# Kernel optimization log

Hardware: AMD Instinct MI355X
Metric: run time of the kernel (lower is better)

The kernel has to match this reference:

```python
import jax, jax.numpy as jnp
import numpy as np

B, T, D = 16, 2048, 64


def setup_inputs() -> dict:
    key = jax.random.key(0)
    kq, kk, kv, kb = jax.random.split(key, 4)
    q = jax.random.normal(kq, (B, T, D), dtype=jnp.float32)
    k = jax.random.normal(kk, (B, T, D), dtype=jnp.float32)
    v = jax.random.normal(kv, (B, T, D), dtype=jnp.float32)
    add_attn = jax.random.normal(kb, (B, T, T), dtype=jnp.float32)
    return {"q": q, "k": k, "v": v, "add_attn": add_attn}


def reference(q, k, v, add_attn):
    # scale = 1/sqrt(head_dim), the standard value passed by callers
    scale = 1.0 / jnp.sqrt(jnp.asarray(q.shape[-1], dtype=q.dtype))
    # [B, T, T] attention logits: bmm(q, k^T) * scale + additive bias
    attn = jnp.einsum('btd,bsd->bts', q, k) * scale + add_attn
    # softmax over keys (dim=2); dropout p=0.0 is identity
    attn = jax.nn.softmax(attn, axis=2)
    # [B, T, D] weighted values
    output = jnp.einsum('bts,bsd->btd', attn, v)
    return (output, attn)
```

## Files before the change

kernel.cpp:

```cpp
#include <hip/hip_runtime.h>
#include <stdint.h>

#define NB 16
#define NT 2048
#define ND 64

typedef __attribute__((ext_vector_type(8))) short bf16x8;
typedef __attribute__((ext_vector_type(4))) float f32x4;
typedef __attribute__((ext_vector_type(4))) _Float16 f16x4;

__device__ __forceinline__ unsigned short f2bf(float f) {
    union { float f; unsigned u; } v; v.f = f;
    unsigned r = v.u + 0x7fffu + ((v.u >> 16) & 1u);
    return (unsigned short)(r >> 16);
}
__device__ __forceinline__ unsigned short f2h(float f) {
    union { _Float16 h; unsigned short u; } v; v.h = (_Float16)f; return v.u;
}

__global__ __launch_bounds__(256) void prep_k(const float* __restrict__ Q,
                                              const float* __restrict__ K,
                                              const float* __restrict__ V,
                                              unsigned short* __restrict__ qbf,
                                              unsigned short* __restrict__ kbf,
                                              unsigned short* __restrict__ vt)
{
    const size_t i = (size_t)blockIdx.x * 256 + threadIdx.x;
    const int which = blockIdx.y;
    if (which == 2) {
        float4 v4 = ((const float4*)V)[i];
        const int d4 = (int)(i & 15);
        const int t  = (int)((i >> 4) & (NT - 1));
        const int b  = (int)(i >> 15);
        unsigned short* base = vt + ((size_t)b * ND + d4 * 4) * NT + t;
        base[0]      = f2h(v4.x);
        base[NT]     = f2h(v4.y);
        base[2 * NT] = f2h(v4.z);
        base[3 * NT] = f2h(v4.w);
    } else {
        const float4* src = (which == 0) ? (const float4*)Q : (const float4*)K;
        unsigned short* dst = (which == 0) ? qbf : kbf;
        float4 v4 = src[i];
        union { unsigned short s[4]; unsigned long long ll; } u;
        u.s[0] = f2bf(v4.x); u.s[1] = f2bf(v4.y);
        u.s[2] = f2bf(v4.z); u.s[3] = f2bf(v4.w);
        *(unsigned long long*)(dst + 4 * i) = u.ll;
    }
}

__global__ __launch_bounds__(256, 2)
void attn_onepass(const unsigned short* __restrict__ qbf,
                  const unsigned short* __restrict__ kbf,
                  const unsigned short* __restrict__ vt,
                  const float* __restrict__ Bias,
                  float* __restrict__ Out,
                  float* __restrict__ Attn)
{
    const int b = blockIdx.y, q0 = blockIdx.x * 16;
    const int tid = threadIdx.x, w = tid >> 6, lane = tid & 63;
    const int n = lane & 15, qd = lane >> 4;
    const int kw0 = w * 512;

    __shared__ float s_rs[4][16];
    __shared__ float s_o[4 * 16 * 68];

    const unsigned short* qp = qbf + ((size_t)(b * NT + q0 + n)) * ND + qd * 8;
    const bf16x8 qf0 = *(const bf16x8*)qp;
    const bf16x8 qf1 = *(const bf16x8*)(qp + 32);
    const float* Bb = Bias + ((size_t)b * NT + q0 + n) * NT;
    float* Ab = Attn + ((size_t)b * NT + q0 + n) * NT;
    const unsigned short* vtb = vt + (size_t)b * ND * NT + (size_t)n * NT;

    f16x4 ev[32];
    float4 bb[4];
    bf16x8 kb0[2], kb1[2];
#pragma unroll
    for (int i = 0; i < 4; ++i)
        bb[i] = *(const float4*)(Bb + kw0 + 16 * i + qd * 4);
#pragma unroll
    for (int i = 0; i < 2; ++i) {
        const unsigned short* kp = kbf + ((size_t)(b * NT + kw0 + 16 * i + n)) * ND + qd * 8;
        kb0[i] = *(const bf16x8*)kp;
        kb1[i] = *(const bf16x8*)(kp + 32);
    }

    float rs = 0.f;
#pragma unroll
    for (int t = 0; t < 32; ++t) {
        const bf16x8 kf0 = kb0[t & 1];
        const bf16x8 kf1 = kb1[t & 1];
        const float4 bs = bb[t & 3];
        if (t + 2 < 32) {
            const unsigned short* kp =
                kbf + ((size_t)(b * NT + kw0 + 16 * (t + 2) + n)) * ND + qd * 8;
            kb0[t & 1] = *(const bf16x8*)kp;
            kb1[t & 1] = *(const bf16x8*)(kp + 32);
        }
        if (t + 4 < 32)
            bb[t & 3] = *(const float4*)(Bb + kw0 + 16 * (t + 4) + qd * 4);
        f32x4 acc = {0.f, 0.f, 0.f, 0.f};
        acc = __builtin_amdgcn_mfma_f32_16x16x32_bf16(kf0, qf0, acc, 0, 0, 0);
        acc = __builtin_amdgcn_mfma_f32_16x16x32_bf16(kf1, qf1, acc, 0, 0, 0);
        float e0 = __expf(__builtin_fmaf(acc[0], 0.125f, bs.x - 2.0f));
        float e1 = __expf(__builtin_fmaf(acc[1], 0.125f, bs.y - 2.0f));
        float e2 = __expf(__builtin_fmaf(acc[2], 0.125f, bs.z - 2.0f));
        float e3 = __expf(__builtin_fmaf(acc[3], 0.125f, bs.w - 2.0f));
        union { _Float16 h[4]; f16x4 v; } u;
        u.h[0] = (_Float16)e0; u.h[1] = (_Float16)e1;
        u.h[2] = (_Float16)e2; u.h[3] = (_Float16)e3;
        ev[t] = u.v;
        rs += (e0 + e1) + (e2 + e3);
    }

    f16x4 vc0[4], vc1[4];
#pragma unroll
    for (int dt = 0; dt < 4; ++dt) {
        const unsigned short* vp = vtb + kw0 + qd * 4 + (size_t)dt * 16 * NT;
        vc0[dt] = *(const f16x4*)(const void*)vp;
        vc1[dt] = *(const f16x4*)(const void*)(vp + 16);
    }

    rs += __shfl_xor(rs, 16, 64);
    rs += __shfl_xor(rs, 32, 64);
    if (lane < 16) s_rs[w][lane] = rs;
    __syncthreads();
    const float tot = (s_rs[0][n] + s_rs[1][n]) + (s_rs[2][n] + s_rs[3][n]);
    const float inv = 1.0f / tot;

    f32x4 oacc[4];
#pragma unroll
    for (int dt = 0; dt < 4; ++dt) oacc[dt] = (f32x4){0.f, 0.f, 0.f, 0.f};

#pragma unroll
    for (int tp = 0; tp < 16; ++tp) {
        const int key0 = kw0 + 32 * tp;
        f16x4 va0[4], va1[4];
#pragma unroll
        for (int dt = 0; dt < 4; ++dt) { va0[dt] = vc0[dt]; va1[dt] = vc1[dt]; }
        if (tp + 1 < 16) {
#pragma unroll
            for (int dt = 0; dt < 4; ++dt) {
                const unsigned short* vp =
                    vtb + key0 + 32 + qd * 4 + (size_t)dt * 16 * NT;
                vc0[dt] = *(const f16x4*)(const void*)vp;
                vc1[dt] = *(const f16x4*)(const void*)(vp + 16);
            }
        }
        const f16x4 e0v = ev[2 * tp];
        const f16x4 e1v = ev[2 * tp + 1];
        float4 s0, s1;
        s0.x = (float)e0v[0] * inv; s0.y = (float)e0v[1] * inv;
        s0.z = (float)e0v[2] * inv; s0.w = (float)e0v[3] * inv;
        s1.x = (float)e1v[0] * inv; s1.y = (float)e1v[1] * inv;
        s1.z = (float)e1v[2] * inv; s1.w = (float)e1v[3] * inv;
        *(float4*)(Ab + key0 + qd * 4) = s0;
        *(float4*)(Ab + key0 + 16 + qd * 4) = s1;
#pragma unroll
        for (int dt = 0; dt < 4; ++dt) {
            oacc[dt] = __builtin_amdgcn_mfma_f32_16x16x16f16(va0[dt], e0v, oacc[dt], 0, 0, 0);
            oacc[dt] = __builtin_amdgcn_mfma_f32_16x16x16f16(va1[dt], e1v, oacc[dt], 0, 0, 0);
        }
    }

#pragma unroll
    for (int dt = 0; dt < 4; ++dt) {
        float4 t4;
        t4.x = oacc[dt][0] * inv; t4.y = oacc[dt][1] * inv;
        t4.z = oacc[dt][2] * inv; t4.w = oacc[dt][3] * inv;
        *(float4*)&s_o[(w * 16 + n) * 68 + dt * 16 + qd * 4] = t4;
    }
    __syncthreads();
    {
        const int row = tid >> 4, d4 = (tid & 15) * 4;
        float4 o0 = *(const float4*)&s_o[(0 * 16 + row) * 68 + d4];
        float4 o1 = *(const float4*)&s_o[(1 * 16 + row) * 68 + d4];
        float4 o2 = *(const float4*)&s_o[(2 * 16 + row) * 68 + d4];
        float4 o3 = *(const float4*)&s_o[(3 * 16 + row) * 68 + d4];
        float4 o;
        o.x = (o0.x + o1.x) + (o2.x + o3.x);
        o.y = (o0.y + o1.y) + (o2.y + o3.y);
        o.z = (o0.z + o1.z) + (o2.z + o3.z);
        o.w = (o0.w + o1.w) + (o2.w + o3.w);
        *(float4*)(Out + ((size_t)b * NT + q0 + row) * ND + d4) = o;
    }
}

__device__ __forceinline__ bf16x8 pack8(float4 a, float4 b) {
    union { unsigned short s[8]; bf16x8 v; } u;
    u.s[0] = f2bf(a.x); u.s[1] = f2bf(a.y); u.s[2] = f2bf(a.z); u.s[3] = f2bf(a.w);
    u.s[4] = f2bf(b.x); u.s[5] = f2bf(b.y); u.s[6] = f2bf(b.z); u.s[7] = f2bf(b.w);
    return u.v;
}
__global__ __launch_bounds__(256, 2)
void attn_fused(const float* __restrict__ Q, const float* __restrict__ K,
                const float* __restrict__ V, const float* __restrict__ Bias,
                float* __restrict__ Out, float* __restrict__ Attn)
{
    const int b  = blockIdx.y;
    const int q0 = blockIdx.x * 16;
    const int tid  = threadIdx.x;
    const int w    = tid >> 6;
    const int lane = tid & 63;
    const int n  = lane & 15;
    const int qd = lane >> 4;
    const int kw0 = w * 512;
    __shared__ float s_rs[4][16];
    __shared__ __align__(16) unsigned char s_rp[4][16 * 80];
    const float* Qb = Q + ((size_t)b * NT + q0) * ND;
    const float* Kb = K + (size_t)b * NT * ND;
    const float* Vb = V + (size_t)b * NT * ND;
    const float* Bb = Bias + ((size_t)b * NT + q0) * NT;
    float* Ab = Attn + ((size_t)b * NT + q0) * NT;
    float* Ob = Out  + ((size_t)b * NT + q0) * ND;
    bf16x8 qf0, qf1;
    {
        const float* qp = Qb + n * ND + qd * 8;
        qf0 = pack8(*(const float4*)qp,        *(const float4*)(qp + 4));
        qf1 = pack8(*(const float4*)(qp + 32), *(const float4*)(qp + 36));
    }
    float ev[32][4];
    float rs = 0.f;
#pragma unroll
    for (int t = 0; t < 32; ++t) {
        const int key0 = kw0 + 16 * t;
        const float* kp = Kb + (size_t)(key0 + n) * ND + qd * 8;
        bf16x8 kf0 = pack8(*(const float4*)kp,        *(const float4*)(kp + 4));
        bf16x8 kf1 = pack8(*(const float4*)(kp + 32), *(const float4*)(kp + 36));
        f32x4 acc = {0.f, 0.f, 0.f, 0.f};
        acc = __builtin_amdgcn_mfma_f32_16x16x32_bf16(kf0, qf0, acc, 0, 0, 0);
        acc = __builtin_amdgcn_mfma_f32_16x16x32_bf16(kf1, qf1, acc, 0, 0, 0);
        float4 bs = *(const float4*)(Bb + (size_t)n * NT + key0 + qd * 4);
        float e0 = __expf(acc[0] * 0.125f + bs.x);
        float e1 = __expf(acc[1] * 0.125f + bs.y);
        float e2 = __expf(acc[2] * 0.125f + bs.z);
        float e3 = __expf(acc[3] * 0.125f + bs.w);
        ev[t][0] = e0; ev[t][1] = e1; ev[t][2] = e2; ev[t][3] = e3;
        rs += (e0 + e1) + (e2 + e3);
    }
    rs += __shfl_xor(rs, 16, 64);
    rs += __shfl_xor(rs, 32, 64);
    if (lane < 16) s_rs[w][lane] = rs;
    __syncthreads();
    const float tot = (s_rs[0][n] + s_rs[1][n]) + (s_rs[2][n] + s_rs[3][n]);
    const float inv = 1.0f / tot;
    f32x4 oacc[4];
#pragma unroll
    for (int dt = 0; dt < 4; ++dt) oacc[dt] = (f32x4){0.f, 0.f, 0.f, 0.f};
    unsigned char* rp = &s_rp[w][0];
#pragma unroll
    for (int c = 0; c < 16; ++c) {
        const int kbase = kw0 + 32 * c;
#pragma unroll
        for (int tt = 0; tt < 2; ++tt) {
            const int t = 2 * c + tt;
            float p0 = ev[t][0] * inv;
            float p1 = ev[t][1] * inv;
            float p2 = ev[t][2] * inv;
            float p3 = ev[t][3] * inv;
            float4 pv; pv.x = p0; pv.y = p1; pv.z = p2; pv.w = p3;
            *(float4*)(Ab + (size_t)n * NT + kbase + 16 * tt + qd * 4) = pv;
            union { unsigned short s[4]; unsigned long long ll; } pu;
            pu.s[0] = f2bf(p0); pu.s[1] = f2bf(p1);
            pu.s[2] = f2bf(p2); pu.s[3] = f2bf(p3);
            *(unsigned long long*)(rp + n * 80 + (16 * tt + 4 * qd) * 2) = pu.ll;
        }
        __syncthreads();
        bf16x8 pf;
        {
            union { uint4 u; bf16x8 v; } uu;
            uu.u = *(const uint4*)(rp + n * 80 + qd * 16);
            pf = uu.v;
        }
#pragma unroll
        for (int dt = 0; dt < 4; ++dt) {
            const int d = dt * 16 + n;
            const float* vp = Vb + (size_t)(kbase + qd * 8) * ND + d;
            float4 va, vb4;
            va.x  = vp[0];   va.y  = vp[64];  va.z  = vp[128]; va.w  = vp[192];
            vb4.x = vp[256]; vb4.y = vp[320]; vb4.z = vp[384]; vb4.w = vp[448];
            bf16x8 vf = pack8(va, vb4);
            oacc[dt] = __builtin_amdgcn_mfma_f32_16x16x32_bf16(vf, pf, oacc[dt], 0, 0, 0);
        }
        __syncthreads();
    }
#pragma unroll
    for (int dt = 0; dt < 4; ++dt)
#pragma unroll
        for (int r = 0; r < 4; ++r)
            atomicAdd(Ob + (size_t)n * ND + dt * 16 + qd * 4 + r, oacc[dt][r]);
}

extern "C" void kernel_launch(void* const* d_in, const int* in_sizes, int n_in,
                              void* d_out, int out_size, void* d_ws, size_t ws_size,
                              hipStream_t stream)
{
    const float* q    = (const float*)d_in[0];
    const float* k    = (const float*)d_in[1];
    const float* v    = (const float*)d_in[2];
    const float* bias = (const float*)d_in[3];
    float* out  = (float*)d_out;
    float* attn = out + (size_t)NB * NT * ND;

    const size_t elems = (size_t)NB * NT * ND;
    const size_t need  = 3 * elems * 2;

    if (ws_size >= need) {
        unsigned short* qbf = (unsigned short*)d_ws;
        unsigned short* kbf = qbf + elems;
        unsigned short* vtb = kbf + elems;
        prep_k<<<dim3((unsigned)(elems / 4 / 256), 3), 256, 0, stream>>>(q, k, v, qbf, kbf, vtb);
        attn_onepass<<<dim3(NT / 16, NB), 256, 0, stream>>>(qbf, kbf, vtb, bias, out, attn);
    } else {
        hipMemsetAsync(out, 0, (size_t)NB * NT * ND * sizeof(float), stream);
        dim3 grid(NT / 16, NB);
        attn_fused<<<grid, 256, 0, stream>>>(q, k, v, bias, out, attn);
    }
}
```

Before: 261.7 us.

## Split key range across 8 waves, remap blocks across XCDs, add sched barriers

Doubles the block to 512 threads, so each of 8 waves handles 256 keys instead of 512. This halves the per-thread exp and V register arrays and raises occupancy. Block indices are permuted so consecutive blocks spread across the 8 XCDs by batch, which changes L2 locality for K/V reuse. Explicit sched_barriers pin where the prefetch loads of K, bias and V sit, and V is now double-buffered two steps ahead. The cost is a larger shared-memory reduction across 8 waves, with half the threads idle in the final sum.

```diff
diff --git a/kernel.cpp b/kernel.cpp
--- a/kernel.cpp
+++ b/kernel.cpp
@@ -48,7 +48,7 @@
     }
 }
 
-__global__ __launch_bounds__(256, 2)
+__global__ __launch_bounds__(512, 4)
 void attn_onepass(const unsigned short* __restrict__ qbf,
                   const unsigned short* __restrict__ kbf,
                   const unsigned short* __restrict__ vt,
@@ -56,13 +56,17 @@
                   float* __restrict__ Out,
                   float* __restrict__ Attn)
 {
-    const int b = blockIdx.y, q0 = blockIdx.x * 16;
+    const int flat = blockIdx.x + (NT / 16) * blockIdx.y;
+    const int lin  = (flat & 7) * 256 + (flat >> 3);
+    const int b    = lin >> 7;
+    const int q0   = (lin & 127) * 16;
+
     const int tid = threadIdx.x, w = tid >> 6, lane = tid & 63;
     const int n = lane & 15, qd = lane >> 4;
-    const int kw0 = w * 512;
-
-    __shared__ float s_rs[4][16];
-    __shared__ float s_o[4 * 16 * 68];
+    const int kw0 = w * 256;
+
+    __shared__ float s_rs[8][16];
+    __shared__ float s_o[8 * 16 * 68];
 
     const unsigned short* qp = qbf + ((size_t)(b * NT + q0 + n)) * ND + qd * 8;
     const bf16x8 qf0 = *(const bf16x8*)qp;
@@ -70,34 +74,29 @@
     const float* Bb = Bias + ((size_t)b * NT + q0 + n) * NT;
     float* Ab = Attn + ((size_t)b * NT + q0 + n) * NT;
     const unsigned short* vtb = vt + (size_t)b * ND * NT + (size_t)n * NT;
-
-    f16x4 ev[32];
+    const unsigned short* kbp = kbf + ((size_t)(b * NT + kw0 + n)) * ND + qd * 8;
+    const float* bbp = Bb + kw0 + qd * 4;
+
+    f16x4 ev[16];
+    bf16x8 kb0[2], kb1[2];
     float4 bb[4];
-    bf16x8 kb0[2], kb1[2];
-#pragma unroll
-    for (int i = 0; i < 4; ++i)
-        bb[i] = *(const float4*)(Bb + kw0 + 16 * i + qd * 4);
 #pragma unroll
     for (int i = 0; i < 2; ++i) {
-        const unsigned short* kp = kbf + ((size_t)(b * NT + kw0 + 16 * i + n)) * ND + qd * 8;
+        const unsigned short* kp = kbp + (size_t)(16 * i) * ND;
         kb0[i] = *(const bf16x8*)kp;
         kb1[i] = *(const bf16x8*)(kp + 32);
     }
+#pragma unroll
+    for (int i = 0; i < 4; ++i)
+        bb[i] = *(const float4*)(bbp + 16 * i);
+    __builtin_amdgcn_sched_barrier(0);
 
     float rs = 0.f;
 #pragma unroll
-    for (int t = 0; t < 32; ++t) {
+    for (int t = 0; t < 16; ++t) {
         const bf16x8 kf0 = kb0[t & 1];
         const bf16x8 kf1 = kb1[t & 1];
         const float4 bs = bb[t & 3];
-        if (t + 2 < 32) {
-            const unsigned short* kp =
-                kbf + ((size_t)(b * NT + kw0 + 16 * (t + 2) + n)) * ND + qd * 8;
-            kb0[t & 1] = *(const bf16x8*)kp;
-            kb1[t & 1] = *(const bf16x8*)(kp + 32);
-        }
-        if (t + 4 < 32)
-            bb[t & 3] = *(const float4*)(Bb + kw0 + 16 * (t + 4) + qd * 4);
         f32x4 acc = {0.f, 0.f, 0.f, 0.f};
         acc = __builtin_amdgcn_mfma_f32_16x16x32_bf16(kf0, qf0, acc, 0, 0, 0);
         acc = __builtin_amdgcn_mfma_f32_16x16x32_bf16(kf1, qf1, acc, 0, 0, 0);
@@ -110,21 +109,34 @@
         u.h[2] = (_Float16)e2; u.h[3] = (_Float16)e3;
         ev[t] = u.v;
         rs += (e0 + e1) + (e2 + e3);
-    }
-
-    f16x4 vc0[4], vc1[4];
-#pragma unroll
-    for (int dt = 0; dt < 4; ++dt) {
-        const unsigned short* vp = vtb + kw0 + qd * 4 + (size_t)dt * 16 * NT;
-        vc0[dt] = *(const f16x4*)(const void*)vp;
-        vc1[dt] = *(const f16x4*)(const void*)(vp + 16);
-    }
+        __builtin_amdgcn_sched_barrier(0);
+        if (t + 2 < 16) {
+            const unsigned short* kp = kbp + (size_t)(16 * (t + 2)) * ND;
+            kb0[t & 1] = *(const bf16x8*)kp;
+            kb1[t & 1] = *(const bf16x8*)(kp + 32);
+        }
+        if (t + 4 < 16)
+            bb[t & 3] = *(const float4*)(bbp + 16 * (t + 4));
+        __builtin_amdgcn_sched_barrier(0);
+    }
+
+    f16x4 vr0[2][4], vr1[2][4];
+#pragma unroll
+    for (int i = 0; i < 2; ++i)
+#pragma unroll
+        for (int dt = 0; dt < 4; ++dt) {
+            const unsigned short* vp = vtb + kw0 + 32 * i + qd * 4 + (size_t)dt * 16 * NT;
+            vr0[i][dt] = *(const f16x4*)(const void*)vp;
+            vr1[i][dt] = *(const f16x4*)(const void*)(vp + 16);
+        }
+    __builtin_amdgcn_sched_barrier(0);
 
     rs += __shfl_xor(rs, 16, 64);
     rs += __shfl_xor(rs, 32, 64);
     if (lane < 16) s_rs[w][lane] = rs;
     __syncthreads();
-    const float tot = (s_rs[0][n] + s_rs[1][n]) + (s_rs[2][n] + s_rs[3][n]);
+    const float tot = ((s_rs[0][n] + s_rs[1][n]) + (s_rs[2][n] + s_rs[3][n])) +
+                      ((s_rs[4][n] + s_rs[5][n]) + (s_rs[6][n] + s_rs[7][n]));
     const float inv = 1.0f / tot;
 
     f32x4 oacc[4];
@@ -132,20 +144,8 @@
     for (int dt = 0; dt < 4; ++dt) oacc[dt] = (f32x4){0.f, 0.f, 0.f, 0.f};
 
 #pragma unroll
-    for (int tp = 0; tp < 16; ++tp) {
+    for (int tp = 0; tp < 8; ++tp) {
         const int key0 = kw0 + 32 * tp;
-        f16x4 va0[4], va1[4];
-#pragma unroll
-        for (int dt = 0; dt < 4; ++dt) { va0[dt] = vc0[dt]; va1[dt] = vc1[dt]; }
-        if (tp + 1 < 16) {
-#pragma unroll
-            for (int dt = 0; dt < 4; ++dt) {
-                const unsigned short* vp =
-                    vtb + key0 + 32 + qd * 4 + (size_t)dt * 16 * NT;
-                vc0[dt] = *(const f16x4*)(const void*)vp;
-                vc1[dt] = *(const f16x4*)(const void*)(vp + 16);
-            }
-        }
         const f16x4 e0v = ev[2 * tp];
         const f16x4 e1v = ev[2 * tp + 1];
         float4 s0, s1;
@@ -157,9 +157,20 @@
         *(float4*)(Ab + key0 + 16 + qd * 4) = s1;
 #pragma unroll
         for (int dt = 0; dt < 4; ++dt) {
-            oacc[dt] = __builtin_amdgcn_mfma_f32_16x16x16f16(va0[dt], e0v, oacc[dt], 0, 0, 0);
-            oacc[dt] = __builtin_amdgcn_mfma_f32_16x16x16f16(va1[dt], e1v, oacc[dt], 0, 0, 0);
-        }
+            oacc[dt] = __builtin_amdgcn_mfma_f32_16x16x16f16(vr0[tp & 1][dt], e0v, oacc[dt], 0, 0, 0);
+            oacc[dt] = __builtin_amdgcn_mfma_f32_16x16x16f16(vr1[tp & 1][dt], e1v, oacc[dt], 0, 0, 0);
+        }
+        __builtin_amdgcn_sched_barrier(0);
+        if (tp + 2 < 8) {
+#pragma unroll
+            for (int dt = 0; dt < 4; ++dt) {
+                const unsigned short* vp =
+                    vtb + kw0 + 32 * (tp + 2) + qd * 4 + (size_t)dt * 16 * NT;
+                vr0[tp & 1][dt] = *(const f16x4*)(const void*)vp;
+                vr1[tp & 1][dt] = *(const f16x4*)(const void*)(vp + 16);
+            }
+        }
+        __builtin_amdgcn_sched_barrier(0);
     }
 
 #pragma unroll
@@ -170,17 +181,21 @@
         *(float4*)&s_o[(w * 16 + n) * 68 + dt * 16 + qd * 4] = t4;
     }
     __syncthreads();
-    {
+    if (tid < 256) {
         const int row = tid >> 4, d4 = (tid & 15) * 4;
         float4 o0 = *(const float4*)&s_o[(0 * 16 + row) * 68 + d4];
         float4 o1 = *(const float4*)&s_o[(1 * 16 + row) * 68 + d4];
         float4 o2 = *(const float4*)&s_o[(2 * 16 + row) * 68 + d4];
         float4 o3 = *(const float4*)&s_o[(3 * 16 + row) * 68 + d4];
+        float4 o4 = *(const float4*)&s_o[(4 * 16 + row) * 68 + d4];
+        float4 o5 = *(const float4*)&s_o[(5 * 16 + row) * 68 + d4];
+        float4 o6 = *(const float4*)&s_o[(6 * 16 + row) * 68 + d4];
+        float4 o7 = *(const float4*)&s_o[(7 * 16 + row) * 68 + d4];
         float4 o;
-        o.x = (o0.x + o1.x) + (o2.x + o3.x);
-        o.y = (o0.y + o1.y) + (o2.y + o3.y);
-        o.z = (o0.z + o1.z) + (o2.z + o3.z);
-        o.w = (o0.w + o1.w) + (o2.w + o3.w);
+        o.x = ((o0.x + o1.x) + (o2.x + o3.x)) + ((o4.x + o5.x) + (o6.x + o7.x));
+        o.y = ((o0.y + o1.y) + (o2.y + o3.y)) + ((o4.y + o5.y) + (o6.y + o7.y));
+        o.z = ((o0.z + o1.z) + (o2.z + o3.z)) + ((o4.z + o5.z) + (o6.z + o7.z));
+        o.w = ((o0.w + o1.w) + (o2.w + o3.w)) + ((o4.w + o5.w) + (o6.w + o7.w));
         *(float4*)(Out + ((size_t)b * NT + q0 + row) * ND + d4) = o;
     }
 }
@@ -309,7 +324,7 @@
         unsigned short* kbf = qbf + elems;
         unsigned short* vtb = kbf + elems;
         prep_k<<<dim3((unsigned)(elems / 4 / 256), 3), 256, 0, stream>>>(q, k, v, qbf, kbf, vtb);
-        attn_onepass<<<dim3(NT / 16, NB), 256, 0, stream>>>(qbf, kbf, vtb, bias, out, attn);
+        attn_onepass<<<dim3(NT / 16, NB), 512, 0, stream>>>(qbf, kbf, vtb, bias, out, attn);
     } else {
         hipMemsetAsync(out, 0, (size_t)NB * NT * ND * sizeof(float), stream);
         dim3 grid(NT / 16, NB);
```

After: 252.2 us. 3.6% less time.
